# Kernel optimization log

Hardware: AMD Instinct MI355X
Metric: run time of the kernel (lower is better)

The kernel has to match this reference:

```python
import jax, jax.numpy as jnp
import numpy as np

NSLICES = 4
HID = 512
IN_FEAT = 342   # input_shape - 1 (last column is phase)
OUT = 311
BATCH = 256


def cubic(y0, y1, y2, y3, mu):
    # Catmull-Rom cubic interpolation, as in the original PFNN code
    return (
        (-0.5 * y0 + 1.5 * y1 - 1.5 * y2 + 0.5 * y3) * mu * mu * mu
        + (y0 - 2.5 * y1 + 2.0 * y2 - 0.5 * y3) * mu * mu
        + (-0.5 * y0 + 0.5 * y2) * mu
        + y1
    )


def setup_inputs() -> dict:
    key = jax.random.key(0)
    ks = jax.random.split(key, 7)
    x = jax.random.uniform(ks[0], (BATCH, IN_FEAT + 1), dtype=jnp.float32)
    s = 0.02
    W0 = jax.random.normal(ks[1], (NSLICES, HID, IN_FEAT), dtype=jnp.float32) * s
    b0 = jax.random.normal(ks[2], (NSLICES, HID), dtype=jnp.float32) * s
    W1 = jax.random.normal(ks[3], (NSLICES, HID, HID), dtype=jnp.float32) * s
    b1 = jax.random.normal(ks[4], (NSLICES, HID), dtype=jnp.float32) * s
    W2 = jax.random.normal(ks[5], (NSLICES, OUT, HID), dtype=jnp.float32) * s
    b2 = jax.random.normal(ks[6], (NSLICES, OUT), dtype=jnp.float32) * s
    return {"x": x, "W0": W0, "b0": b0, "W1": W1, "b1": b1, "W2": W2, "b2": b2}


def reference(x, W0, b0, W1, b1, W2, b2):
    phase = x[:, -1]                       # [B]
    pscale = NSLICES * phase
    mu = jnp.mod(pscale, 1.0)              # [B]
    i1 = jnp.floor(pscale).astype(jnp.int32) % NSLICES
    i0 = (i1 - 1) % NSLICES
    i2 = (i1 + 1) % NSLICES
    i3 = (i1 + 2) % NSLICES
    muW = mu[:, None, None]                # broadcast over (out, in)
    mub = mu[:, None]

    Wb0 = cubic(W0[i0], W0[i1], W0[i2], W0[i3], muW)   # [B, 512, 342]
    bb0 = cubic(b0[i0], b0[i1], b0[i2], b0[i3], mub)   # [B, 512]
    Wb1 = cubic(W1[i0], W1[i1], W1[i2], W1[i3], muW)   # [B, 512, 512]
    bb1 = cubic(b1[i0], b1[i1], b1[i2], b1[i3], mub)
    Wb2 = cubic(W2[i0], W2[i1], W2[i2], W2[i3], muW)   # [B, 311, 512]
    bb2 = cubic(b2[i0], b2[i1], b2[i2], b2[i3], mub)

    h = x[:, :-1]                                       # [B, 342]
    h = jax.nn.elu(jnp.einsum('boi,bi->bo', Wb0, h) + bb0)
    h = jax.nn.elu(jnp.einsum('boi,bi->bo', Wb1, h) + bb1)
    out = jnp.einsum('boi,bi->bo', Wb2, h) + bb2        # [B, 311]
    return out
```

## Files before the change

kernel.cpp:

```cpp
#include <hip/hip_runtime.h>
#include <math.h>

#define HID 512
#define IN_FEAT 342
#define OUTD 311
#define BATCH 256
#define KP0 352
#define XROW (IN_FEAT + 1)
#define NB 16
#define NTHR 256

#define NT0 32
#define NCC0 11
#define NT1 32
#define NCC1 16
#define NT2 20
#define NCC2 16

typedef unsigned short u16;
typedef short bf16x8 __attribute__((ext_vector_type(8)));
typedef float f32x4 __attribute__((ext_vector_type(4)));

__device__ __forceinline__ u16 f2bf_rne(float v) {
    unsigned int x = __float_as_uint(v);
    unsigned int r = (x + 0x7fffu + ((x >> 16) & 1u)) >> 16;
    return (u16)r;
}
__device__ __forceinline__ float bf2f(u16 u) {
    return __uint_as_float(((unsigned int)u) << 16);
}

union U8 { u16 u[8]; uint4 v; };

__device__ __forceinline__ void split8(const float* __restrict__ src, bf16x8& hi, bf16x8& lo) {
#pragma unroll
    for (int j = 0; j < 8; j++) {
        u16 h = f2bf_rne(src[j]);
        hi[j] = (short)h;
        lo[j] = (short)f2bf_rne(src[j] - bf2f(h));
    }
}

__global__ __launch_bounds__(256) void prep_frag(
    const float* __restrict__ W0, const float* __restrict__ W1, const float* __restrict__ W2,
    u16* __restrict__ F0, u16* __restrict__ F1, u16* __restrict__ F2)
{
    __shared__ u16 fr[16 * 1024];
    const int bid = (int)blockIdx.x;
    const int tid = (int)threadIdx.x;

    if (bid < 128) {
        const int s = bid >> 5, ot = bid & 31;
        for (int idx = tid; idx < 16 * 44; idx += 256) {
            int rr = idx / 44, c = idx - rr * 44;
            int k = c * 8;
            const float* rp = W0 + (size_t)(s * 512 + ot * 16 + rr) * IN_FEAT;
            float src[8];
            if (k + 8 <= IN_FEAT) {
                const float2* p2 = reinterpret_cast<const float2*>(rp + k);
                float2 v0 = p2[0], v1 = p2[1], v2 = p2[2], v3 = p2[3];
                src[0] = v0.x; src[1] = v0.y; src[2] = v1.x; src[3] = v1.y;
                src[4] = v2.x; src[5] = v2.y; src[6] = v3.x; src[7] = v3.y;
            } else {
#pragma unroll
                for (int j = 0; j < 8; j++) src[j] = (k + j < IN_FEAT) ? rp[k + j] : 0.f;
            }
            U8 hi, lo;
#pragma unroll
            for (int j = 0; j < 8; j++) {
                u16 h = f2bf_rne(src[j]);
                hi.u[j] = h;
                lo.u[j] = f2bf_rne(src[j] - bf2f(h));
            }
            int cc = c >> 2, lane = (c & 3) * 16 + rr;
            *reinterpret_cast<uint4*>(&fr[cc * 1024 + lane * 8])       = hi.v;
            *reinterpret_cast<uint4*>(&fr[cc * 1024 + 512 + lane * 8]) = lo.v;
        }
        __syncthreads();
        uint4* dst = reinterpret_cast<uint4*>(F0 + (size_t)(s * NT0 + ot) * NCC0 * 1024);
        const uint4* srcp = reinterpret_cast<const uint4*>(fr);
        for (int idx = tid; idx < NCC0 * 128; idx += 256) dst[idx] = srcp[idx];
    } else if (bid < 256) {
        const int l = bid - 128;
        const int s = l >> 5, ot = l & 31;
        for (int idx = tid; idx < 16 * 64; idx += 256) {
            int rr = idx >> 6, c = idx & 63;
            const float4* p4 = reinterpret_cast<const float4*>(
                W1 + (size_t)(s * 512 + ot * 16 + rr) * 512 + c * 8);
            float4 v0 = p4[0], v1 = p4[1];
            float src[8] = {v0.x, v0.y, v0.z, v0.w, v1.x, v1.y, v1.z, v1.w};
            U8 hi, lo;
#pragma unroll
            for (int j = 0; j < 8; j++) {
                u16 h = f2bf_rne(src[j]);
                hi.u[j] = h;
                lo.u[j] = f2bf_rne(src[j] - bf2f(h));
            }
            int cc = c >> 2, lane = (c & 3) * 16 + rr;
            *reinterpret_cast<uint4*>(&fr[cc * 1024 + lane * 8])       = hi.v;
            *reinterpret_cast<uint4*>(&fr[cc * 1024 + 512 + lane * 8]) = lo.v;
        }
        __syncthreads();
        uint4* dst = reinterpret_cast<uint4*>(F1 + (size_t)(s * NT1 + ot) * NCC1 * 1024);
        const uint4* srcp = reinterpret_cast<const uint4*>(fr);
        for (int idx = tid; idx < NCC1 * 128; idx += 256) dst[idx] = srcp[idx];
    } else {
        const int l = bid - 256;
        const int s = l / 20, ot = l - s * 20;
        for (int idx = tid; idx < 16 * 64; idx += 256) {
            int rr = idx >> 6, c = idx & 63;
            int orow = ot * 16 + rr;
            float src[8] = {0.f, 0.f, 0.f, 0.f, 0.f, 0.f, 0.f, 0.f};
            if (orow < OUTD) {
                const float4* p4 = reinterpret_cast<const float4*>(
                    W2 + ((size_t)s * OUTD + orow) * 512 + c * 8);
                float4 v0 = p4[0], v1 = p4[1];
                src[0] = v0.x; src[1] = v0.y; src[2] = v0.z; src[3] = v0.w;
                src[4] = v1.x; src[5] = v1.y; src[6] = v1.z; src[7] = v1.w;
            }
            U8 hi, lo;
#pragma unroll
            for (int j = 0; j < 8; j++) {
                u16 h = f2bf_rne(src[j]);
                hi.u[j] = h;
                lo.u[j] = f2bf_rne(src[j] - bf2f(h));
            }
            int cc = c >> 2, lane = (c & 3) * 16 + rr;
            *reinterpret_cast<uint4*>(&fr[cc * 1024 + lane * 8])       = hi.v;
            *reinterpret_cast<uint4*>(&fr[cc * 1024 + 512 + lane * 8]) = lo.v;
        }
        __syncthreads();
        uint4* dst = reinterpret_cast<uint4*>(F2 + (size_t)(s * NT2 + ot) * NCC2 * 1024);
        const uint4* srcp = reinterpret_cast<const uint4*>(fr);
        for (int idx = tid; idx < NCC2 * 128; idx += 256) dst[idx] = srcp[idx];
    }
}

template<int KP, int KLDS, int FINAL, int MODE, int NT, int NBY>
__global__ __launch_bounds__(NTHR, 4) void layer_frag(
    const u16* __restrict__ Wf, const float* __restrict__ x,
    const u16* __restrict__ Hhi, const u16* __restrict__ Hlo,
    const float* __restrict__ bias, int Mb,
    u16* __restrict__ Ohi, u16* __restrict__ Olo, float* __restrict__ outp)
{
    union SharedU {
        u16 h[2][NB * KLDS];
        float acc[4][NB][17];
    };
    __shared__ SharedU sm;

    const int blk = (int)blockIdx.x;
    const int bx = (blk >> 3) & 15;
    const int by = (blk & 7) | ((blk >> 7) << 3);
    if (by >= NBY) return;

    const int tid = (int)threadIdx.x;
    const int b0 = bx * NB;
    const int o0 = by * 16;

    constexpr int CH = KP / 8;
    if constexpr (MODE == 0) {
        for (int idx = tid; idx < NB * CH; idx += NTHR) {
            int r = idx / CH, c = idx - r * CH;
            int k = c * 8;
            const float* xr = x + (size_t)(b0 + r) * XROW;
            float src[8];
#pragma unroll
            for (int j = 0; j < 8; j++) {
                int kk = k + j;
                src[j] = (kk < IN_FEAT) ? xr[kk] : 0.f;
            }
            bf16x8 hi, lo;
            split8(src, hi, lo);
            *reinterpret_cast<bf16x8*>(&sm.h[0][r * KLDS + k]) = hi;
            *reinterpret_cast<bf16x8*>(&sm.h[1][r * KLDS + k]) = lo;
        }
    } else {
        for (int idx = tid; idx < NB * CH; idx += NTHR) {
            int r = idx / CH, c = idx - r * CH;
            size_t g = (size_t)(b0 + r) * KP + c * 8;
            *reinterpret_cast<uint4*>(&sm.h[0][r * KLDS + c * 8]) =
                *reinterpret_cast<const uint4*>(Hhi + g);
            *reinterpret_cast<uint4*>(&sm.h[1][r * KLDS + c * 8]) =
                *reinterpret_cast<const uint4*>(Hlo + g);
        }
    }
    __syncthreads();

    const int lane = tid & 63;
    const int s = tid >> 6;
    const int m = lane & 15;
    const int q = lane >> 4;

    constexpr int NCC = KP / 32;
    const u16* wf = Wf + ((size_t)(s * NT + by) * NCC) * 1024 + lane * 8;
    const u16* hp  = &sm.h[0][m * KLDS + q * 8];
    const u16* hpl = &sm.h[1][m * KLDS + q * 8];

    const int brow = b0 + m;
    const float ps = 4.f * x[(size_t)brow * XROW + IN_FEAT];
    const float fl = floorf(ps);
    const float mu = ps - fl;
    const int i1 = ((int)fl) & 3;
    const int jj = (s - i1) & 3;
    const float mu2 = mu * mu, mu3 = mu2 * mu;
    const float ds = (jj == 0) ? ( 1.5f * mu3 - 2.5f * mu2 + 1.0f)
                   : (jj == 1) ? (-1.5f * mu3 + 2.0f * mu2 + 0.5f * mu)
                   : (jj == 2) ? ( 0.5f * mu3 - 0.5f * mu2)
                   :             (-0.5f * mu3 + mu2 - 0.5f * mu);

    f32x4 a0 = {0.f, 0.f, 0.f, 0.f};
    f32x4 a1 = {0.f, 0.f, 0.f, 0.f};
    f32x4 a2 = {0.f, 0.f, 0.f, 0.f};
#pragma unroll
    for (int cc = 0; cc < NCC; ++cc) {
        bf16x8 ah = *reinterpret_cast<const bf16x8*>(wf + cc * 1024);
        bf16x8 al = *reinterpret_cast<const bf16x8*>(wf + cc * 1024 + 512);
        bf16x8 bh = *reinterpret_cast<const bf16x8*>(hp + cc * 32);
        bf16x8 bl = *reinterpret_cast<const bf16x8*>(hpl + cc * 32);
        a0 = __builtin_amdgcn_mfma_f32_16x16x32_bf16(ah, bh, a0, 0, 0, 0);
        a1 = __builtin_amdgcn_mfma_f32_16x16x32_bf16(ah, bl, a1, 0, 0, 0);
        a2 = __builtin_amdgcn_mfma_f32_16x16x32_bf16(al, bh, a2, 0, 0, 0);
    }
    __syncthreads();

    f32x4 sum = a0 + a1 + a2;
#pragma unroll
    for (int r = 0; r < 4; ++r) {
        int o = o0 + q * 4 + r;
        float bb = (o < Mb) ? bias[(size_t)s * Mb + o] : 0.f;
        sm.acc[s][m][q * 4 + r] = ds * (sum[r] + bb);
    }
    __syncthreads();

    const int b_l = tid >> 4;
    const int o_l = tid & 15;
    float vv = sm.acc[0][b_l][o_l] + sm.acc[1][b_l][o_l]
             + sm.acc[2][b_l][o_l] + sm.acc[3][b_l][o_l];
    const int o = o0 + o_l;
    const int b = b0 + b_l;
    if (!FINAL) {
        float e = (vv > 0.f) ? vv : expm1f(vv);
        u16 h = f2bf_rne(e);
        Ohi[(size_t)b * HID + o] = h;
        Olo[(size_t)b * HID + o] = f2bf_rne(e - bf2f(h));
    } else if (o < OUTD) {
        outp[(size_t)b * OUTD + o] = vv;
    }
}

extern "C" void kernel_launch(void* const* d_in, const int* in_sizes, int n_in,
                              void* d_out, int out_size, void* d_ws, size_t ws_size,
                              hipStream_t stream) {
    const float* x  = (const float*)d_in[0];
    const float* W0 = (const float*)d_in[1];
    const float* b0v = (const float*)d_in[2];
    const float* W1 = (const float*)d_in[3];
    const float* b1v = (const float*)d_in[4];
    const float* W2 = (const float*)d_in[5];
    const float* b2v = (const float*)d_in[6];
    float* out = (float*)d_out;

    char* pw = (char*)d_ws;
    auto alloc = [&](size_t bytes) { char* r = pw; pw += (bytes + 255) & ~(size_t)255; return r; };

    u16* F0 = (u16*)alloc((size_t)4 * NT0 * NCC0 * 1024 * 2);
    u16* F1 = (u16*)alloc((size_t)4 * NT1 * NCC1 * 1024 * 2);
    u16* F2 = (u16*)alloc((size_t)4 * NT2 * NCC2 * 1024 * 2);
    u16* hahi = (u16*)alloc((size_t)BATCH * HID * 2);
    u16* halo = (u16*)alloc((size_t)BATCH * HID * 2);
    u16* hbhi = (u16*)alloc((size_t)BATCH * HID * 2);
    u16* hblo = (u16*)alloc((size_t)BATCH * HID * 2);

    prep_frag<<<336, 256, 0, stream>>>(W0, W1, W2, F0, F1, F2);

    layer_frag<KP0, 360, 0, 0, NT0, 32><<<512, NTHR, 0, stream>>>(
        F0, x, nullptr, nullptr, b0v, HID, hahi, halo, nullptr);

    layer_frag<HID, 520, 0, 1, NT1, 32><<<512, NTHR, 0, stream>>>(
        F1, x, hahi, halo, b1v, HID, hbhi, hblo, nullptr);

    layer_frag<HID, 520, 1, 1, NT2, 20><<<384, NTHR, 0, stream>>>(
        F2, x, hbhi, hblo, b2v, OUTD, nullptr, nullptr, out);
}
```

Baseline: 99.56 us.

## Fuse W0 fragment prep into layer-0 kernel and piggyback W1/W2 prep

Removes the separate prep_frag launch. The new layer0_fused kernel converts its own W0 tile straight into LDS as hi/lo bf16 fragments and runs layer 0 on 32-row batch tiles with 512 threads. The first 208 blocks then also convert the W1/W2 fragments into global buffers for the later layers. This saves one launch and the F0 global round trip. In exchange, each of the 8 batch-tile blocks sharing an output tile redoes the W0 conversion, and LDS use rises to about 136 KB per block, which may limit occupancy.

```diff
diff --git a/kernel.cpp b/kernel.cpp
--- a/kernel.cpp
+++ b/kernel.cpp
@@ -7,15 +7,12 @@
 #define BATCH 256
 #define KP0 352
 #define XROW (IN_FEAT + 1)
-#define NB 16
-#define NTHR 256
-
-#define NT0 32
-#define NCC0 11
+
 #define NT1 32
 #define NCC1 16
 #define NT2 20
 #define NCC2 16
+#define NCC0 11
 
 typedef unsigned short u16;
 typedef short bf16x8 __attribute__((ext_vector_type(8)));
@@ -41,29 +38,155 @@
     }
 }
 
-__global__ __launch_bounds__(256) void prep_frag(
+#define NB0 32
+#define KLDS0 360
+__global__ __launch_bounds__(512, 1) void layer0_fused(
     const float* __restrict__ W0, const float* __restrict__ W1, const float* __restrict__ W2,
-    u16* __restrict__ F0, u16* __restrict__ F1, u16* __restrict__ F2)
+    const float* __restrict__ x, const float* __restrict__ bias,
+    u16* __restrict__ F1, u16* __restrict__ F2,
+    u16* __restrict__ Ohi, u16* __restrict__ Olo)
 {
-    __shared__ u16 fr[16 * 1024];
-    const int bid = (int)blockIdx.x;
+    __shared__ u16 wlds[4 * NCC0 * 1024];
+    __shared__ u16 hlds[2 * NB0 * KLDS0];
+    __shared__ float accs[4][NB0][17];
+
+    const int blk = (int)blockIdx.x;
+    const int bx = (blk >> 3) & 7;
+    const int by = (blk & 7) | ((blk >> 6) << 3);
     const int tid = (int)threadIdx.x;
-
-    if (bid < 128) {
-        const int s = bid >> 5, ot = bid & 31;
-        for (int idx = tid; idx < 16 * 44; idx += 256) {
-            int rr = idx / 44, c = idx - rr * 44;
-            int k = c * 8;
-            const float* rp = W0 + (size_t)(s * 512 + ot * 16 + rr) * IN_FEAT;
-            float src[8];
-            if (k + 8 <= IN_FEAT) {
-                const float2* p2 = reinterpret_cast<const float2*>(rp + k);
-                float2 v0 = p2[0], v1 = p2[1], v2 = p2[2], v3 = p2[3];
-                src[0] = v0.x; src[1] = v0.y; src[2] = v1.x; src[3] = v1.y;
-                src[4] = v2.x; src[5] = v2.y; src[6] = v3.x; src[7] = v3.y;
+    const int b0 = bx * NB0;
+    const int o0 = by * 16;
+
+    for (int idx = tid; idx < 4 * 16 * 44; idx += 512) {
+        int s = idx / (16 * 44);
+        int rem = idx - s * (16 * 44);
+        int rr = rem / 44, c = rem - rr * 44;
+        int k = c * 8;
+        const float* rp = W0 + (size_t)(s * 512 + o0 + rr) * IN_FEAT;
+        float src[8];
+        if (k + 8 <= IN_FEAT) {
+            const float2* p2 = reinterpret_cast<const float2*>(rp + k);
+            float2 v0 = p2[0], v1 = p2[1], v2 = p2[2], v3 = p2[3];
+            src[0] = v0.x; src[1] = v0.y; src[2] = v1.x; src[3] = v1.y;
+            src[4] = v2.x; src[5] = v2.y; src[6] = v3.x; src[7] = v3.y;
+        } else {
+#pragma unroll
+            for (int j = 0; j < 8; j++) src[j] = (k + j < IN_FEAT) ? rp[k + j] : 0.f;
+        }
+        U8 hi, lo;
+#pragma unroll
+        for (int j = 0; j < 8; j++) {
+            u16 h = f2bf_rne(src[j]);
+            hi.u[j] = h;
+            lo.u[j] = f2bf_rne(src[j] - bf2f(h));
+        }
+        int cc = c >> 2, lane = (c & 3) * 16 + rr;
+        *reinterpret_cast<uint4*>(&wlds[(s * NCC0 + cc) * 1024 + lane * 8])       = hi.v;
+        *reinterpret_cast<uint4*>(&wlds[(s * NCC0 + cc) * 1024 + 512 + lane * 8]) = lo.v;
+    }
+
+    for (int idx = tid; idx < NB0 * 44; idx += 512) {
+        int r = idx / 44, c = idx - r * 44;
+        int k = c * 8;
+        const float* xr = x + (size_t)(b0 + r) * XROW;
+        float src[8];
+#pragma unroll
+        for (int j = 0; j < 8; j++) {
+            int kk = k + j;
+            src[j] = (kk < IN_FEAT) ? xr[kk] : 0.f;
+        }
+        bf16x8 hi, lo;
+        split8(src, hi, lo);
+        *reinterpret_cast<bf16x8*>(&hlds[r * KLDS0 + k])                 = hi;
+        *reinterpret_cast<bf16x8*>(&hlds[NB0 * KLDS0 + r * KLDS0 + k])   = lo;
+    }
+    __syncthreads();
+
+    const int lane = tid & 63;
+    const int w = tid >> 6;
+    const int s = w & 3;
+    const int t = w >> 2;
+    const int m = lane & 15;
+    const int q = lane >> 4;
+
+    const u16* wf  = &wlds[s * NCC0 * 1024 + lane * 8];
+    const u16* hp  = &hlds[(t * 16 + m) * KLDS0 + q * 8];
+    const u16* hpl = &hlds[NB0 * KLDS0 + (t * 16 + m) * KLDS0 + q * 8];
+
+    const int brow = b0 + t * 16 + m;
+    const float ps = 4.f * x[(size_t)brow * XROW + IN_FEAT];
+    const float fl = floorf(ps);
+    const float mu = ps - fl;
+    const int i1 = ((int)fl) & 3;
+    const int jj = (s - i1) & 3;
+    const float mu2 = mu * mu, mu3 = mu2 * mu;
+    const float ds = (jj == 0) ? ( 1.5f * mu3 - 2.5f * mu2 + 1.0f)
+                   : (jj == 1) ? (-1.5f * mu3 + 2.0f * mu2 + 0.5f * mu)
+                   : (jj == 2) ? ( 0.5f * mu3 - 0.5f * mu2)
+                   :             (-0.5f * mu3 + mu2 - 0.5f * mu);
+
+    f32x4 a0 = {0.f, 0.f, 0.f, 0.f};
+    f32x4 a1 = {0.f, 0.f, 0.f, 0.f};
+    f32x4 a2 = {0.f, 0.f, 0.f, 0.f};
+#pragma unroll
+    for (int cc = 0; cc < NCC0; ++cc) {
+        bf16x8 ah = *reinterpret_cast<const bf16x8*>(wf + cc * 1024);
+        bf16x8 al = *reinterpret_cast<const bf16x8*>(wf + cc * 1024 + 512);
+        bf16x8 bh = *reinterpret_cast<const bf16x8*>(hp + cc * 32);
+        bf16x8 bl = *reinterpret_cast<const bf16x8*>(hpl + cc * 32);
+        a0 = __builtin_amdgcn_mfma_f32_16x16x32_bf16(ah, bh, a0, 0, 0, 0);
+        a1 = __builtin_amdgcn_mfma_f32_16x16x32_bf16(ah, bl, a1, 0, 0, 0);
+        a2 = __builtin_amdgcn_mfma_f32_16x16x32_bf16(al, bh, a2, 0, 0, 0);
+    }
+    __syncthreads();
+
+    f32x4 sum = a0 + a1 + a2;
+#pragma unroll
+    for (int r = 0; r < 4; ++r) {
+        int o = o0 + q * 4 + r;
+        accs[s][t * 16 + m][q * 4 + r] = ds * (sum[r] + bias[(size_t)s * HID + o]);
+    }
+    __syncthreads();
+
+    const int b_l = tid >> 4;
+    const int o_l = tid & 15;
+    float vv = accs[0][b_l][o_l] + accs[1][b_l][o_l]
+             + accs[2][b_l][o_l] + accs[3][b_l][o_l];
+    {
+        float e = (vv > 0.f) ? vv : expm1f(vv);
+        u16 h = f2bf_rne(e);
+        const int o = o0 + o_l;
+        const int b = b0 + b_l;
+        Ohi[(size_t)b * HID + o] = h;
+        Olo[(size_t)b * HID + o] = f2bf_rne(e - bf2f(h));
+    }
+
+    if (blk < 208) {
+        const bool w2j = (blk >= 128);
+        int l = w2j ? (blk - 128) : blk;
+        int js, jot;
+        if (w2j) { js = l / 20; jot = l - js * 20; }
+        else     { js = l >> 5; jot = l & 31; }
+        u16* Fd = w2j ? (F2 + (size_t)(js * NT2 + jot) * NCC2 * 1024)
+                      : (F1 + (size_t)(js * NT1 + jot) * NCC1 * 1024);
+        for (int idx = tid; idx < 16 * 64; idx += 512) {
+            int rr = idx >> 6, c = idx & 63;
+            float src[8] = {0.f, 0.f, 0.f, 0.f, 0.f, 0.f, 0.f, 0.f};
+            if (!w2j) {
+                const float4* p4 = reinterpret_cast<const float4*>(
+                    W1 + (size_t)(js * 512 + jot * 16 + rr) * 512 + c * 8);
+                float4 v0 = p4[0], v1 = p4[1];
+                src[0] = v0.x; src[1] = v0.y; src[2] = v0.z; src[3] = v0.w;
+                src[4] = v1.x; src[5] = v1.y; src[6] = v1.z; src[7] = v1.w;
             } else {
-#pragma unroll
-                for (int j = 0; j < 8; j++) src[j] = (k + j < IN_FEAT) ? rp[k + j] : 0.f;
+                int orow = jot * 16 + rr;
+                if (orow < OUTD) {
+                    const float4* p4 = reinterpret_cast<const float4*>(
+                        W2 + ((size_t)js * OUTD + orow) * 512 + c * 8);
+                    float4 v0 = p4[0], v1 = p4[1];
+                    src[0] = v0.x; src[1] = v0.y; src[2] = v0.z; src[3] = v0.w;
+                    src[4] = v1.x; src[5] = v1.y; src[6] = v1.z; src[7] = v1.w;
+                }
             }
             U8 hi, lo;
 #pragma unroll
@@ -72,71 +195,16 @@
                 hi.u[j] = h;
                 lo.u[j] = f2bf_rne(src[j] - bf2f(h));
             }
-            int cc = c >> 2, lane = (c & 3) * 16 + rr;
-            *reinterpret_cast<uint4*>(&fr[cc * 1024 + lane * 8])       = hi.v;
-            *reinterpret_cast<uint4*>(&fr[cc * 1024 + 512 + lane * 8]) = lo.v;
+            int cc = c >> 2, jl = (c & 3) * 16 + rr;
+            *reinterpret_cast<uint4*>(Fd + cc * 1024 + jl * 8)       = hi.v;
+            *reinterpret_cast<uint4*>(Fd + cc * 1024 + 512 + jl * 8) = lo.v;
         }
-        __syncthreads();
-        uint4* dst = reinterpret_cast<uint4*>(F0 + (size_t)(s * NT0 + ot) * NCC0 * 1024);
-        const uint4* srcp = reinterpret_cast<const uint4*>(fr);
-        for (int idx = tid; idx < NCC0 * 128; idx += 256) dst[idx] = srcp[idx];
-    } else if (bid < 256) {
-        const int l = bid - 128;
-        const int s = l >> 5, ot = l & 31;
-        for (int idx = tid; idx < 16 * 64; idx += 256) {
-            int rr = idx >> 6, c = idx & 63;
-            const float4* p4 = reinterpret_cast<const float4*>(
-                W1 + (size_t)(s * 512 + ot * 16 + rr) * 512 + c * 8);
-            float4 v0 = p4[0], v1 = p4[1];
-            float src[8] = {v0.x, v0.y, v0.z, v0.w, v1.x, v1.y, v1.z, v1.w};
-            U8 hi, lo;
-#pragma unroll
-            for (int j = 0; j < 8; j++) {
-                u16 h = f2bf_rne(src[j]);
-                hi.u[j] = h;
-                lo.u[j] = f2bf_rne(src[j] - bf2f(h));
-            }
-            int cc = c >> 2, lane = (c & 3) * 16 + rr;
-            *reinterpret_cast<uint4*>(&fr[cc * 1024 + lane * 8])       = hi.v;
-            *reinterpret_cast<uint4*>(&fr[cc * 1024 + 512 + lane * 8]) = lo.v;
-        }
-        __syncthreads();
-        uint4* dst = reinterpret_cast<uint4*>(F1 + (size_t)(s * NT1 + ot) * NCC1 * 1024);
-        const uint4* srcp = reinterpret_cast<const uint4*>(fr);
-        for (int idx = tid; idx < NCC1 * 128; idx += 256) dst[idx] = srcp[idx];
-    } else {
-        const int l = bid - 256;
-        const int s = l / 20, ot = l - s * 20;
-        for (int idx = tid; idx < 16 * 64; idx += 256) {
-            int rr = idx >> 6, c = idx & 63;
-            int orow = ot * 16 + rr;
-            float src[8] = {0.f, 0.f, 0.f, 0.f, 0.f, 0.f, 0.f, 0.f};
-            if (orow < OUTD) {
-                const float4* p4 = reinterpret_cast<const float4*>(
-                    W2 + ((size_t)s * OUTD + orow) * 512 + c * 8);
-                float4 v0 = p4[0], v1 = p4[1];
-                src[0] = v0.x; src[1] = v0.y; src[2] = v0.z; src[3] = v0.w;
-                src[4] = v1.x; src[5] = v1.y; src[6] = v1.z; src[7] = v1.w;
-            }
-            U8 hi, lo;
-#pragma unroll
-            for (int j = 0; j < 8; j++) {
-                u16 h = f2bf_rne(src[j]);
-                hi.u[j] = h;
-                lo.u[j] = f2bf_rne(src[j] - bf2f(h));
-            }
-            int cc = c >> 2, lane = (c & 3) * 16 + rr;
-            *reinterpret_cast<uint4*>(&fr[cc * 1024 + lane * 8])       = hi.v;
-            *reinterpret_cast<uint4*>(&fr[cc * 1024 + 512 + lane * 8]) = lo.v;
-        }
-        __syncthreads();
-        uint4* dst = reinterpret_cast<uint4*>(F2 + (size_t)(s * NT2 + ot) * NCC2 * 1024);
-        const uint4* srcp = reinterpret_cast<const uint4*>(fr);
-        for (int idx = tid; idx < NCC2 * 128; idx += 256) dst[idx] = srcp[idx];
-    }
-}
-
-template<int KP, int KLDS, int FINAL, int MODE, int NT, int NBY>
+    }
+}
+
+#define NB 16
+#define NTHR 256
+template<int KP, int KLDS, int FINAL, int NT, int NBY>
 __global__ __launch_bounds__(NTHR, 4) void layer_frag(
     const u16* __restrict__ Wf, const float* __restrict__ x,
     const u16* __restrict__ Hhi, const u16* __restrict__ Hlo,
@@ -159,31 +227,13 @@
     const int o0 = by * 16;
 
     constexpr int CH = KP / 8;
-    if constexpr (MODE == 0) {
-        for (int idx = tid; idx < NB * CH; idx += NTHR) {
-            int r = idx / CH, c = idx - r * CH;
-            int k = c * 8;
-            const float* xr = x + (size_t)(b0 + r) * XROW;
-            float src[8];
-#pragma unroll
-            for (int j = 0; j < 8; j++) {
-                int kk = k + j;
-                src[j] = (kk < IN_FEAT) ? xr[kk] : 0.f;
-            }
-            bf16x8 hi, lo;
-            split8(src, hi, lo);
-            *reinterpret_cast<bf16x8*>(&sm.h[0][r * KLDS + k]) = hi;
-            *reinterpret_cast<bf16x8*>(&sm.h[1][r * KLDS + k]) = lo;
-        }
-    } else {
-        for (int idx = tid; idx < NB * CH; idx += NTHR) {
-            int r = idx / CH, c = idx - r * CH;
-            size_t g = (size_t)(b0 + r) * KP + c * 8;
-            *reinterpret_cast<uint4*>(&sm.h[0][r * KLDS + c * 8]) =
-                *reinterpret_cast<const uint4*>(Hhi + g);
-            *reinterpret_cast<uint4*>(&sm.h[1][r * KLDS + c * 8]) =
-                *reinterpret_cast<const uint4*>(Hlo + g);
-        }
+    for (int idx = tid; idx < NB * CH; idx += NTHR) {
+        int r = idx / CH, c = idx - r * CH;
+        size_t g = (size_t)(b0 + r) * KP + c * 8;
+        *reinterpret_cast<uint4*>(&sm.h[0][r * KLDS + c * 8]) =
+            *reinterpret_cast<const uint4*>(Hhi + g);
+        *reinterpret_cast<uint4*>(&sm.h[1][r * KLDS + c * 8]) =
+            *reinterpret_cast<const uint4*>(Hlo + g);
     }
     __syncthreads();
 
@@ -264,7 +314,6 @@
     char* pw = (char*)d_ws;
     auto alloc = [&](size_t bytes) { char* r = pw; pw += (bytes + 255) & ~(size_t)255; return r; };
 
-    u16* F0 = (u16*)alloc((size_t)4 * NT0 * NCC0 * 1024 * 2);
     u16* F1 = (u16*)alloc((size_t)4 * NT1 * NCC1 * 1024 * 2);
     u16* F2 = (u16*)alloc((size_t)4 * NT2 * NCC2 * 1024 * 2);
     u16* hahi = (u16*)alloc((size_t)BATCH * HID * 2);
@@ -272,14 +321,12 @@
     u16* hbhi = (u16*)alloc((size_t)BATCH * HID * 2);
     u16* hblo = (u16*)alloc((size_t)BATCH * HID * 2);
 
-    prep_frag<<<336, 256, 0, stream>>>(W0, W1, W2, F0, F1, F2);
-
-    layer_frag<KP0, 360, 0, 0, NT0, 32><<<512, NTHR, 0, stream>>>(
-        F0, x, nullptr, nullptr, b0v, HID, hahi, halo, nullptr);
-
-    layer_frag<HID, 520, 0, 1, NT1, 32><<<512, NTHR, 0, stream>>>(
+    layer0_fused<<<256, 512, 0, stream>>>(
+        W0, W1, W2, x, b0v, F1, F2, hahi, halo);
+
+    layer_frag<HID, 520, 0, NT1, 32><<<512, NTHR, 0, stream>>>(
         F1, x, hahi, halo, b1v, HID, hbhi, hblo, nullptr);
 
-    layer_frag<HID, 520, 1, 1, NT2, 20><<<384, NTHR, 0, stream>>>(
+    layer_frag<HID, 520, 1, NT2, 20><<<384, NTHR, 0, stream>>>(
         F2, x, hbhi, hblo, b2v, OUTD, nullptr, nullptr, out);
 }
```

New measurement: 100.7 us. No clear change (+1.1%).
